# Performance work log

Hardware: AMD Instinct MI355X
Metric: run time of the kernel (lower is better)

The kernel has to match this reference:

```python
import jax, jax.numpy as jnp
import numpy as np

B, T, D, H, HD = 4, 2048, 1024, 16, 64
EPS = 1e-6


def _rotary_tables(seq_len, d_head):
    n = d_head // 4
    angular_freq = (1.0 / 1024) ** jnp.linspace(0, 1, n, dtype=jnp.float32)
    angular_freq = jnp.concatenate([angular_freq, jnp.zeros((n,), jnp.float32)])  # [d_head//2]
    theta = jnp.outer(jnp.arange(seq_len, dtype=jnp.float32), angular_freq)  # [T, d_head//2]
    return jnp.cos(theta), jnp.sin(theta)


def _apply_rotary(x, cos, sin):
    # x: [B, T, H, d]
    xf = x.astype(jnp.float32)
    x1, x2 = jnp.split(xf, 2, axis=-1)
    c = cos[None, :, None, :]
    s = sin[None, :, None, :]
    y1 = x1 * c + x2 * s
    y2 = -x1 * s + x2 * c
    return jnp.concatenate([y1, y2], axis=-1).astype(x.dtype)


def _rmsnorm(x, eps):
    return x * jax.lax.rsqrt(jnp.mean(x * x, axis=-1, keepdims=True) + eps)


def setup_inputs() -> dict:
    key = jax.random.key(0)
    ks = jax.random.split(key, 5)
    scale = 1.0 / np.sqrt(D)
    x = jax.random.normal(ks[0], (B, T, D), jnp.float32)
    wq = jax.random.normal(ks[1], (D, D), jnp.float32) * scale
    wk = jax.random.normal(ks[2], (D, D), jnp.float32) * scale
    wv = jax.random.normal(ks[3], (D, D), jnp.float32) * scale
    wo = jax.random.normal(ks[4], (D, D), jnp.float32) * scale
    mask = jnp.tril(jnp.ones((T, T), dtype=bool))  # causal
    return {"x": x, "wq": wq, "wk": wk, "wv": wv, "wo": wo, "mask": mask}


def reference(x, wq, wk, wv, wo, mask):
    # QKV projections (equinox Linear: y = x @ W.T)
    q = (x @ wq.T).reshape(B, T, H, HD)
    k = (x @ wk.T).reshape(B, T, H, HD)
    v = (x @ wv.T).reshape(B, T, H, HD)
    # QK-norm (RMS norm without weight)
    q = _rmsnorm(q, EPS)
    k = _rmsnorm(k, EPS)
    # Rotary embedding
    cos, sin = _rotary_tables(T, HD)
    q = _apply_rotary(q, cos, sin)
    k = _apply_rotary(k, cos, sin)
    # Attention
    scores = jnp.einsum('bshd,bthd->bhst', q, k) / jnp.sqrt(jnp.float32(HD))
    scores = jnp.where(mask[None, None, :, :], scores, -jnp.inf)
    weights = jax.nn.softmax(scores, axis=-1)
    out = jnp.einsum('bhst,bthd->bshd', weights, v)
    out = out.reshape(B, T, D)
    return out @ wo.T
```

## Files before the change

kernel.cpp:

```cpp
#include <hip/hip_runtime.h>
#include <hip/hip_bf16.h>
#include <math.h>

#define B_ 4
#define T_ 2048
#define D_ 1024
#define H_ 16
#define HD_ 64

typedef _Float16 f16x8 __attribute__((ext_vector_type(8)));
typedef _Float16 f16x4 __attribute__((ext_vector_type(4)));
typedef float f32x4 __attribute__((ext_vector_type(4)));

__device__ __forceinline__ void gload_lds16(const _Float16* g, _Float16* l) {
    __builtin_amdgcn_global_load_lds(
        (const __attribute__((address_space(1))) void*)g,
        (__attribute__((address_space(3))) void*)l,
        16, 0, 0);
}

__global__ __launch_bounds__(256) void castf(const float* __restrict__ in,
                                             _Float16* __restrict__ out, int n4) {
    const int i = blockIdx.x * 256 + threadIdx.x;
    if (i < n4) {
        const float4 v = ((const float4*)in)[i];
        f16x4 h = {(_Float16)v.x, (_Float16)v.y, (_Float16)v.z, (_Float16)v.w};
        ((f16x4*)out)[i] = h;
    }
}

__global__ __launch_bounds__(256) void castw(const float* __restrict__ a,
                                             const float* __restrict__ b,
                                             const float* __restrict__ c,
                                             const float* __restrict__ d,
                                             _Float16* __restrict__ oa,
                                             _Float16* __restrict__ ob,
                                             _Float16* __restrict__ oc,
                                             _Float16* __restrict__ od) {
    const int z = blockIdx.z;
    const float* in = (z == 0) ? a : (z == 1 ? b : (z == 2 ? c : d));
    _Float16* out = (z == 0) ? oa : (z == 1 ? ob : (z == 2 ? oc : od));
    const int i = blockIdx.x * 256 + threadIdx.x;
    const float4 v = ((const float4*)in)[i];
    f16x4 h = {(_Float16)v.x, (_Float16)v.y, (_Float16)v.z, (_Float16)v.w};
    ((f16x4*)out)[i] = h;
}

__global__ __launch_bounds__(256) void gemm_qkv(const _Float16* __restrict__ A,
                                                const _Float16* __restrict__ Wq,
                                                const _Float16* __restrict__ Wk,
                                                const _Float16* __restrict__ Wv,
                                                _Float16* __restrict__ qh,
                                                _Float16* __restrict__ kh,
                                                _Float16* __restrict__ vt) {
    constexpr int K = D_;
    const int z = blockIdx.z;
    const _Float16* W = (z == 0) ? Wq : (z == 1 ? Wk : Wv);
    __shared__ _Float16 As[128 * 32];
    __shared__ _Float16 Bs[128 * 32];
    const int tid = threadIdx.x;
    const int lane = tid & 63, w = tid >> 6;
    const int col = lane & 15, quad = lane >> 4;
    const int wm = w >> 1, wn = w & 1;
    const int row0 = blockIdx.x * 128, col0 = blockIdx.y * 128;
    const int sr = lane >> 2, sc = (lane & 3) * 8;

    f32x4 acc[4][4];
#pragma unroll
    for (int i = 0; i < 4; ++i)
#pragma unroll
        for (int j = 0; j < 4; ++j) acc[i][j] = (f32x4){0.f, 0.f, 0.f, 0.f};

    for (int kt = 0; kt < K / 32; ++kt) {
        const int k0 = kt * 32;
#pragma unroll
        for (int it = 0; it < 2; ++it) {
            const int rb = it * 64 + w * 16;
            gload_lds16(A + (size_t)(row0 + rb + sr) * K + k0 + sc, As + rb * 32);
            gload_lds16(W + (size_t)(col0 + rb + sr) * K + k0 + sc, Bs + rb * 32);
        }
        __syncthreads();
        f16x8 af[4], bf[4];
#pragma unroll
        for (int i = 0; i < 4; ++i) {
            af[i] = *(const f16x8*)&As[(wm * 64 + i * 16 + col) * 32 + quad * 8];
            bf[i] = *(const f16x8*)&Bs[(wn * 64 + i * 16 + col) * 32 + quad * 8];
        }
#pragma unroll
        for (int mi = 0; mi < 4; ++mi)
#pragma unroll
            for (int ni = 0; ni < 4; ++ni)
                acc[mi][ni] = __builtin_amdgcn_mfma_f32_16x16x32_f16(af[mi], bf[ni],
                                                                     acc[mi][ni], 0, 0, 0);
        __syncthreads();
    }

    if (z < 2) {
        _Float16* C = (z == 0) ? qh : kh;
        const float qscale = (z == 0) ? 0.18033688011112042f : 1.0f;
        const float fr = exp2f(-10.0f * (float)col * (1.0f / 15.0f));
#pragma unroll
        for (int mi = 0; mi < 4; ++mi) {
            float ssq[4];
#pragma unroll
            for (int r = 0; r < 4; ++r) {
                float t = 0.f;
#pragma unroll
                for (int ni = 0; ni < 4; ++ni) t += acc[mi][ni][r] * acc[mi][ni][r];
                ssq[r] = t;
            }
#pragma unroll
            for (int st = 1; st < 16; st <<= 1)
#pragma unroll
                for (int r = 0; r < 4; ++r) ssq[r] += __shfl_xor(ssq[r], st, 64);
            const int rowb = row0 + wm * 64 + mi * 16 + quad * 4;
#pragma unroll
            for (int r = 0; r < 4; ++r) {
                const float scl = rsqrtf(ssq[r] * (1.0f / 64.0f) + 1e-6f) * qscale;
                const int t = (rowb + r) & (T_ - 1);
                float s, c;
                __sincosf((float)t * fr, &s, &c);
                const float x0 = acc[mi][0][r] * scl;
                const float x1 = acc[mi][1][r] * scl;
                const float x2 = acc[mi][2][r] * scl;
                const float x3 = acc[mi][3][r] * scl;
                const float y0 = fmaf(x0, c, x2 * s);
                const float y2 = fmaf(x2, c, -x0 * s);
                const size_t base = (size_t)(rowb + r) * D_ + col0 + wn * 64 + col;
                C[base + 0]  = (_Float16)y0;
                C[base + 16] = (_Float16)x1;
                C[base + 32] = (_Float16)y2;
                C[base + 48] = (_Float16)x3;
            }
        }
    } else {
        const int hh = blockIdx.y * 2 + wn;
#pragma unroll
        for (int mi = 0; mi < 4; ++mi) {
            const int row = row0 + wm * 64 + mi * 16 + quad * 4;
            const int bb = row >> 11;
            const int t0m = row & (T_ - 1);
#pragma unroll
            for (int ni = 0; ni < 4; ++ni) {
                const int d = ni * 16 + col;
                f16x4 pk = {(_Float16)acc[mi][ni][0], (_Float16)acc[mi][ni][1],
                            (_Float16)acc[mi][ni][2], (_Float16)acc[mi][ni][3]};
                *(f16x4*)&vt[((size_t)(bb * H_ + hh) * HD_ + d) * T_ + t0m] = pk;
            }
        }
    }
}

__global__ __launch_bounds__(256) void gemm_wo(const _Float16* __restrict__ A,
                                               const _Float16* __restrict__ W,
                                               float* __restrict__ C) {
    constexpr int K = D_, N = D_;
    __shared__ _Float16 As[128 * 32];
    __shared__ _Float16 Bs[128 * 32];
    const int tid = threadIdx.x;
    const int lane = tid & 63, w = tid >> 6;
    const int col = lane & 15, quad = lane >> 4;
    const int wm = w >> 1, wn = w & 1;
    const int row0 = blockIdx.x * 128, col0 = blockIdx.y * 128;
    const int sr = lane >> 2, sc = (lane & 3) * 8;

    f32x4 acc[4][4];
#pragma unroll
    for (int i = 0; i < 4; ++i)
#pragma unroll
        for (int j = 0; j < 4; ++j) acc[i][j] = (f32x4){0.f, 0.f, 0.f, 0.f};

    for (int kt = 0; kt < K / 32; ++kt) {
        const int k0 = kt * 32;
#pragma unroll
        for (int it = 0; it < 2; ++it) {
            const int rb = it * 64 + w * 16;
            gload_lds16(A + (size_t)(row0 + rb + sr) * K + k0 + sc, As + rb * 32);
            gload_lds16(W + (size_t)(col0 + rb + sr) * K + k0 + sc, Bs + rb * 32);
        }
        __syncthreads();
        f16x8 af[4], bf[4];
#pragma unroll
        for (int i = 0; i < 4; ++i) {
            af[i] = *(const f16x8*)&As[(wm * 64 + i * 16 + col) * 32 + quad * 8];
            bf[i] = *(const f16x8*)&Bs[(wn * 64 + i * 16 + col) * 32 + quad * 8];
        }
#pragma unroll
        for (int mi = 0; mi < 4; ++mi)
#pragma unroll
            for (int ni = 0; ni < 4; ++ni)
                acc[mi][ni] = __builtin_amdgcn_mfma_f32_16x16x32_f16(af[mi], bf[ni],
                                                                     acc[mi][ni], 0, 0, 0);
        __syncthreads();
    }
#pragma unroll
    for (int mi = 0; mi < 4; ++mi)
#pragma unroll
        for (int ni = 0; ni < 4; ++ni)
#pragma unroll
            for (int r = 0; r < 4; ++r)
                C[(size_t)(row0 + wm * 64 + mi * 16 + quad * 4 + r) * N +
                  col0 + wn * 64 + ni * 16 + col] = acc[mi][ni][r];
}

#define LDP 88

__global__ __launch_bounds__(512) void flash_mfma(const _Float16* __restrict__ qh,
                                                  const _Float16* __restrict__ kh,
                                                  const _Float16* __restrict__ vt,
                                                  _Float16* __restrict__ o) {
    __shared__ _Float16 Kl[2][64 * 64];
    __shared__ _Float16 Vl[2][64 * 64];
    __shared__ _Float16 Pl[8][16 * LDP];
    const int tid = threadIdx.x;
    const int lane = tid & 63, w = tid >> 6;
    const int col = lane & 15, quad = lane >> 4;
    const int bh = blockIdx.x, b = bh >> 4, h = bh & 15;
    const int srow = lane >> 3;
    const int schunk = (lane & 7) ^ srow;
    const int sw = col & 7;
    const int sr = w * 8 + srow;
    const _Float16* kbase = kh + ((size_t)(b * T_ + sr) * H_ + h) * HD_ + schunk * 8;
    const _Float16* vbase = vt + ((size_t)(b * H_ + h) * HD_ + sr) * T_ + schunk * 8;

    for (int phase = 0; phase < 2; ++phase) {
        const int qt = (phase == 0) ? (int)blockIdx.y : (15 - (int)blockIdx.y);
        const int q0 = qt * 128;

        const int tq = q0 + w * 16 + col;
        const _Float16* qp = qh + ((size_t)(b * T_ + tq) * H_ + h) * HD_ + quad * 8;
        const f16x8 qB0 = *(const f16x8*)(qp);
        const f16x8 qB1 = *(const f16x8*)(qp + 32);

        f32x4 oa[4];
#pragma unroll
        for (int i = 0; i < 4; ++i) oa[i] = (f32x4){0.f, 0.f, 0.f, 0.f};
        float l_ = 0.f;

        const int nkt = 2 * qt + 2;
        gload_lds16(kbase, Kl[0] + (w * 8) * 64);
        gload_lds16(vbase, Vl[0] + (w * 8) * 64);

        for (int kt = 0; kt < nkt; ++kt) {
            const int cur = kt & 1;
            __syncthreads();
            if (kt + 1 < nkt) {
                const int k1 = (kt + 1) * 64;
                gload_lds16(kbase + (size_t)k1 * D_, Kl[cur ^ 1] + (w * 8) * 64);
                gload_lds16(vbase + k1, Vl[cur ^ 1] + (w * 8) * 64);
            }
            const int k0 = kt * 64;

            f32x4 s[4];
#pragma unroll
            for (int tn = 0; tn < 4; ++tn) {
                const _Float16* kp = &Kl[cur][(tn * 16 + col) * 64];
                const f16x8 kA0 = *(const f16x8*)(kp + ((quad ^ sw) << 3));
                const f16x8 kA1 = *(const f16x8*)(kp + (((quad | 4) ^ sw) << 3));
                f32x4 a = (f32x4){0.f, 0.f, 0.f, 0.f};
                a = __builtin_amdgcn_mfma_f32_16x16x32_f16(kA0, qB0, a, 0, 0, 0);
                a = __builtin_amdgcn_mfma_f32_16x16x32_f16(kA1, qB1, a, 0, 0, 0);
                s[tn] = a;
            }

            if (k0 + 63 > q0 + w * 16) {
                const int qq = q0 + w * 16 + col;
#pragma unroll
                for (int tn = 0; tn < 4; ++tn)
#pragma unroll
                    for (int r = 0; r < 4; ++r) {
                        const int key = k0 + tn * 16 + quad * 4 + r;
                        if (key > qq) s[tn][r] = -1e30f;
                    }
            }

#pragma unroll
            for (int tn = 0; tn < 4; ++tn) {
                f16x4 pk;
#pragma unroll
                for (int r = 0; r < 4; ++r) {
                    const float p = exp2f(s[tn][r]);
                    l_ += p;
                    pk[r] = (_Float16)p;
                }
                *(f16x4*)&Pl[w][col * LDP + tn * 16 + quad * 4] = pk;
            }

            const f16x8 pA0 = *(const f16x8*)&Pl[w][col * LDP + quad * 8];
            const f16x8 pA1 = *(const f16x8*)&Pl[w][col * LDP + quad * 8 + 32];
#pragma unroll
            for (int tn = 0; tn < 4; ++tn) {
                const _Float16* vp = &Vl[cur][(tn * 16 + col) * 64];
                const f16x8 vB0 = *(const f16x8*)(vp + ((quad ^ sw) << 3));
                const f16x8 vB1 = *(const f16x8*)(vp + (((quad | 4) ^ sw) << 3));
                oa[tn] = __builtin_amdgcn_mfma_f32_16x16x32_f16(pA0, vB0, oa[tn], 0, 0, 0);
                oa[tn] = __builtin_amdgcn_mfma_f32_16x16x32_f16(pA1, vB1, oa[tn], 0, 0, 0);
            }
        }
        __syncthreads();

        l_ += __shfl_xor(l_, 16, 64);
        l_ += __shfl_xor(l_, 32, 64);
        const float linv = 1.0f / l_;
        float inv[4];
#pragma unroll
        for (int r = 0; r < 4; ++r) inv[r] = __shfl(linv, quad * 4 + r, 64);
#pragma unroll
        for (int tn = 0; tn < 4; ++tn)
#pragma unroll
            for (int r = 0; r < 4; ++r)
                o[((size_t)(b * T_ + q0 + w * 16 + quad * 4 + r) * H_ + h) * HD_ + tn * 16 + col] =
                    (_Float16)(oa[tn][r] * inv[r]);
    }
}

extern "C" void kernel_launch(void* const* d_in, const int* in_sizes, int n_in,
                              void* d_out, int out_size, void* d_ws, size_t ws_size,
                              hipStream_t stream) {
    const float* x  = (const float*)d_in[0];
    const float* wq = (const float*)d_in[1];
    const float* wk = (const float*)d_in[2];
    const float* wv = (const float*)d_in[3];
    const float* wo = (const float*)d_in[4];
    float* out = (float*)d_out;

    const size_t NE = (size_t)B_ * T_ * D_;
    const size_t WE = (size_t)D_ * D_;
    _Float16* xh  = (_Float16*)d_ws;
    _Float16* qh  = xh + NE;
    _Float16* kh  = qh + NE;
    _Float16* vth = kh + NE;
    _Float16* oh  = vth + NE;
    _Float16* wqh = oh + NE;
    _Float16* wkh = wqh + WE;
    _Float16* wvh = wkh + WE;
    _Float16* woh = wvh + WE;

    castf<<<NE / 1024, 256, 0, stream>>>(x, xh, (int)(NE / 4));
    castw<<<dim3(WE / 1024, 1, 4), 256, 0, stream>>>(wq, wk, wv, wo,
                                                     wqh, wkh, wvh, woh);

    gemm_qkv<<<dim3((B_ * T_) / 128, D_ / 128, 3), 256, 0, stream>>>(
        xh, wqh, wkh, wvh, qh, kh, vth);

    flash_mfma<<<dim3(B_ * H_, 8, 1), 512, 0, stream>>>(qh, kh, vth, oh);

    gemm_wo<<<dim3((B_ * T_) / 128, D_ / 128, 1), 256, 0, stream>>>(oh, woh, out);
}
```

Measured before the change: 280.5 us.

## Restructure flash attention to 4 waves with 32 query rows each

The flash kernel moves from 512-thread blocks, each processing two paired causal query tiles, to 256-thread blocks that each own one 128-row query tile, launched longest-first. Each wave now computes two 16-row query sub-tiles, so every K/V fragment read from LDS feeds twice as many MFMAs. The double-buffered K/V prefetch is dropped for a single buffer loaded and synchronised each iteration. The intent is more data reuse per LDS read and more blocks per CU, at the cost of losing load/compute overlap within a block and of the paired-tile load balancing.

```diff
diff --git a/kernel.cpp b/kernel.cpp
--- a/kernel.cpp
+++ b/kernel.cpp
@@ -205,113 +205,134 @@
 
 #define LDP 88
 
-__global__ __launch_bounds__(512) void flash_mfma(const _Float16* __restrict__ qh,
+__global__ __launch_bounds__(256) void flash_mfma(const _Float16* __restrict__ qh,
                                                   const _Float16* __restrict__ kh,
                                                   const _Float16* __restrict__ vt,
                                                   _Float16* __restrict__ o) {
-    __shared__ _Float16 Kl[2][64 * 64];
-    __shared__ _Float16 Vl[2][64 * 64];
-    __shared__ _Float16 Pl[8][16 * LDP];
+    __shared__ _Float16 Kl[64 * 64];
+    __shared__ _Float16 Vl[64 * 64];
+    __shared__ _Float16 Pl[4][32 * LDP];
     const int tid = threadIdx.x;
     const int lane = tid & 63, w = tid >> 6;
     const int col = lane & 15, quad = lane >> 4;
     const int bh = blockIdx.x, b = bh >> 4, h = bh & 15;
+    const int qt = 15 - (int)blockIdx.y;
+    const int q0 = qt * 128;
     const int srow = lane >> 3;
-    const int schunk = (lane & 7) ^ srow;
+    const int schunk = ((lane & 7) ^ srow) * 8;
     const int sw = col & 7;
-    const int sr = w * 8 + srow;
-    const _Float16* kbase = kh + ((size_t)(b * T_ + sr) * H_ + h) * HD_ + schunk * 8;
-    const _Float16* vbase = vt + ((size_t)(b * H_ + h) * HD_ + sr) * T_ + schunk * 8;
-
-    for (int phase = 0; phase < 2; ++phase) {
-        const int qt = (phase == 0) ? (int)blockIdx.y : (15 - (int)blockIdx.y);
-        const int q0 = qt * 128;
-
-        const int tq = q0 + w * 16 + col;
-        const _Float16* qp = qh + ((size_t)(b * T_ + tq) * H_ + h) * HD_ + quad * 8;
-        const f16x8 qB0 = *(const f16x8*)(qp);
-        const f16x8 qB1 = *(const f16x8*)(qp + 32);
-
-        f32x4 oa[4];
-#pragma unroll
-        for (int i = 0; i < 4; ++i) oa[i] = (f32x4){0.f, 0.f, 0.f, 0.f};
-        float l_ = 0.f;
-
-        const int nkt = 2 * qt + 2;
-        gload_lds16(kbase, Kl[0] + (w * 8) * 64);
-        gload_lds16(vbase, Vl[0] + (w * 8) * 64);
-
-        for (int kt = 0; kt < nkt; ++kt) {
-            const int cur = kt & 1;
-            __syncthreads();
-            if (kt + 1 < nkt) {
-                const int k1 = (kt + 1) * 64;
-                gload_lds16(kbase + (size_t)k1 * D_, Kl[cur ^ 1] + (w * 8) * 64);
-                gload_lds16(vbase + k1, Vl[cur ^ 1] + (w * 8) * 64);
+
+    const int qa = q0 + w * 32 + col;
+    const _Float16* qpa = qh + ((size_t)(b * T_ + qa) * H_ + h) * HD_ + quad * 8;
+    const f16x8 qB0a = *(const f16x8*)(qpa);
+    const f16x8 qB1a = *(const f16x8*)(qpa + 32);
+    const _Float16* qpb = qpa + (size_t)16 * D_;
+    const f16x8 qB0b = *(const f16x8*)(qpb);
+    const f16x8 qB1b = *(const f16x8*)(qpb + 32);
+
+    f32x4 oaa[4], oab[4];
+#pragma unroll
+    for (int i = 0; i < 4; ++i) {
+        oaa[i] = (f32x4){0.f, 0.f, 0.f, 0.f};
+        oab[i] = (f32x4){0.f, 0.f, 0.f, 0.f};
+    }
+    float la = 0.f, lb = 0.f;
+
+    const int nkt = 2 * qt + 2;
+    for (int kt = 0; kt < nkt; ++kt) {
+        const int k0 = kt * 64;
+#pragma unroll
+        for (int half = 0; half < 2; ++half) {
+            const int r = half * 32 + w * 8 + srow;
+            gload_lds16(kh + ((size_t)(b * T_ + k0 + r) * H_ + h) * HD_ + schunk,
+                        Kl + (half * 32 + w * 8) * 64);
+            gload_lds16(vt + ((size_t)(b * H_ + h) * HD_ + r) * T_ + k0 + schunk,
+                        Vl + (half * 32 + w * 8) * 64);
+        }
+        __syncthreads();
+
+        f32x4 sa[4], sb[4];
+#pragma unroll
+        for (int tn = 0; tn < 4; ++tn) {
+            const _Float16* kp = &Kl[(tn * 16 + col) * 64];
+            const f16x8 kA0 = *(const f16x8*)(kp + ((quad ^ sw) << 3));
+            const f16x8 kA1 = *(const f16x8*)(kp + (((quad | 4) ^ sw) << 3));
+            f32x4 xa = (f32x4){0.f, 0.f, 0.f, 0.f};
+            f32x4 xb = (f32x4){0.f, 0.f, 0.f, 0.f};
+            xa = __builtin_amdgcn_mfma_f32_16x16x32_f16(kA0, qB0a, xa, 0, 0, 0);
+            xb = __builtin_amdgcn_mfma_f32_16x16x32_f16(kA0, qB0b, xb, 0, 0, 0);
+            xa = __builtin_amdgcn_mfma_f32_16x16x32_f16(kA1, qB1a, xa, 0, 0, 0);
+            xb = __builtin_amdgcn_mfma_f32_16x16x32_f16(kA1, qB1b, xb, 0, 0, 0);
+            sa[tn] = xa;
+            sb[tn] = xb;
+        }
+
+        if (k0 + 63 > q0 + w * 32) {
+#pragma unroll
+            for (int tn = 0; tn < 4; ++tn)
+#pragma unroll
+                for (int r = 0; r < 4; ++r) {
+                    const int key = k0 + tn * 16 + quad * 4 + r;
+                    if (key > qa) sa[tn][r] = -1e30f;
+                    if (key > qa + 16) sb[tn][r] = -1e30f;
+                }
+        }
+
+#pragma unroll
+        for (int tn = 0; tn < 4; ++tn) {
+            f16x4 pka, pkb;
+#pragma unroll
+            for (int r = 0; r < 4; ++r) {
+                const float pa = exp2f(sa[tn][r]);
+                const float pb = exp2f(sb[tn][r]);
+                la += pa;
+                lb += pb;
+                pka[r] = (_Float16)pa;
+                pkb[r] = (_Float16)pb;
             }
-            const int k0 = kt * 64;
-
-            f32x4 s[4];
-#pragma unroll
-            for (int tn = 0; tn < 4; ++tn) {
-                const _Float16* kp = &Kl[cur][(tn * 16 + col) * 64];
-                const f16x8 kA0 = *(const f16x8*)(kp + ((quad ^ sw) << 3));
-                const f16x8 kA1 = *(const f16x8*)(kp + (((quad | 4) ^ sw) << 3));
-                f32x4 a = (f32x4){0.f, 0.f, 0.f, 0.f};
-                a = __builtin_amdgcn_mfma_f32_16x16x32_f16(kA0, qB0, a, 0, 0, 0);
-                a = __builtin_amdgcn_mfma_f32_16x16x32_f16(kA1, qB1, a, 0, 0, 0);
-                s[tn] = a;
-            }
-
-            if (k0 + 63 > q0 + w * 16) {
-                const int qq = q0 + w * 16 + col;
-#pragma unroll
-                for (int tn = 0; tn < 4; ++tn)
-#pragma unroll
-                    for (int r = 0; r < 4; ++r) {
-                        const int key = k0 + tn * 16 + quad * 4 + r;
-                        if (key > qq) s[tn][r] = -1e30f;
-                    }
-            }
-
-#pragma unroll
-            for (int tn = 0; tn < 4; ++tn) {
-                f16x4 pk;
-#pragma unroll
-                for (int r = 0; r < 4; ++r) {
-                    const float p = exp2f(s[tn][r]);
-                    l_ += p;
-                    pk[r] = (_Float16)p;
-                }
-                *(f16x4*)&Pl[w][col * LDP + tn * 16 + quad * 4] = pk;
-            }
-
-            const f16x8 pA0 = *(const f16x8*)&Pl[w][col * LDP + quad * 8];
-            const f16x8 pA1 = *(const f16x8*)&Pl[w][col * LDP + quad * 8 + 32];
-#pragma unroll
-            for (int tn = 0; tn < 4; ++tn) {
-                const _Float16* vp = &Vl[cur][(tn * 16 + col) * 64];
-                const f16x8 vB0 = *(const f16x8*)(vp + ((quad ^ sw) << 3));
-                const f16x8 vB1 = *(const f16x8*)(vp + (((quad | 4) ^ sw) << 3));
-                oa[tn] = __builtin_amdgcn_mfma_f32_16x16x32_f16(pA0, vB0, oa[tn], 0, 0, 0);
-                oa[tn] = __builtin_amdgcn_mfma_f32_16x16x32_f16(pA1, vB1, oa[tn], 0, 0, 0);
-            }
-        }
-        __syncthreads();
-
-        l_ += __shfl_xor(l_, 16, 64);
-        l_ += __shfl_xor(l_, 32, 64);
-        const float linv = 1.0f / l_;
-        float inv[4];
-#pragma unroll
-        for (int r = 0; r < 4; ++r) inv[r] = __shfl(linv, quad * 4 + r, 64);
-#pragma unroll
-        for (int tn = 0; tn < 4; ++tn)
-#pragma unroll
-            for (int r = 0; r < 4; ++r)
-                o[((size_t)(b * T_ + q0 + w * 16 + quad * 4 + r) * H_ + h) * HD_ + tn * 16 + col] =
-                    (_Float16)(oa[tn][r] * inv[r]);
-    }
+            *(f16x4*)&Pl[w][col * LDP + tn * 16 + quad * 4] = pka;
+            *(f16x4*)&Pl[w][(col + 16) * LDP + tn * 16 + quad * 4] = pkb;
+        }
+
+        const f16x8 pA0a = *(const f16x8*)&Pl[w][col * LDP + quad * 8];
+        const f16x8 pA1a = *(const f16x8*)&Pl[w][col * LDP + quad * 8 + 32];
+        const f16x8 pA0b = *(const f16x8*)&Pl[w][(col + 16) * LDP + quad * 8];
+        const f16x8 pA1b = *(const f16x8*)&Pl[w][(col + 16) * LDP + quad * 8 + 32];
+#pragma unroll
+        for (int tn = 0; tn < 4; ++tn) {
+            const _Float16* vp = &Vl[(tn * 16 + col) * 64];
+            const f16x8 vB0 = *(const f16x8*)(vp + ((quad ^ sw) << 3));
+            const f16x8 vB1 = *(const f16x8*)(vp + (((quad | 4) ^ sw) << 3));
+            oaa[tn] = __builtin_amdgcn_mfma_f32_16x16x32_f16(pA0a, vB0, oaa[tn], 0, 0, 0);
+            oab[tn] = __builtin_amdgcn_mfma_f32_16x16x32_f16(pA0b, vB0, oab[tn], 0, 0, 0);
+            oaa[tn] = __builtin_amdgcn_mfma_f32_16x16x32_f16(pA1a, vB1, oaa[tn], 0, 0, 0);
+            oab[tn] = __builtin_amdgcn_mfma_f32_16x16x32_f16(pA1b, vB1, oab[tn], 0, 0, 0);
+        }
+        __syncthreads();
+    }
+
+    la += __shfl_xor(la, 16, 64);
+    la += __shfl_xor(la, 32, 64);
+    lb += __shfl_xor(lb, 16, 64);
+    lb += __shfl_xor(lb, 32, 64);
+    const float linva = 1.0f / la;
+    const float linvb = 1.0f / lb;
+    float inva[4], invb[4];
+#pragma unroll
+    for (int r = 0; r < 4; ++r) {
+        inva[r] = __shfl(linva, quad * 4 + r, 64);
+        invb[r] = __shfl(linvb, quad * 4 + r, 64);
+    }
+    const int qrow = q0 + w * 32 + quad * 4;
+#pragma unroll
+    for (int tn = 0; tn < 4; ++tn)
+#pragma unroll
+        for (int r = 0; r < 4; ++r) {
+            o[((size_t)(b * T_ + qrow + r) * H_ + h) * HD_ + tn * 16 + col] =
+                (_Float16)(oaa[tn][r] * inva[r]);
+            o[((size_t)(b * T_ + qrow + 16 + r) * H_ + h) * HD_ + tn * 16 + col] =
+                (_Float16)(oab[tn][r] * invb[r]);
+        }
 }
 
 extern "C" void kernel_launch(void* const* d_in, const int* in_sizes, int n_in,
@@ -343,7 +364,7 @@
     gemm_qkv<<<dim3((B_ * T_) / 128, D_ / 128, 3), 256, 0, stream>>>(
         xh, wqh, wkh, wvh, qh, kh, vth);
 
-    flash_mfma<<<dim3(B_ * H_, 8, 1), 512, 0, stream>>>(qh, kh, vth, oh);
+    flash_mfma<<<dim3(B_ * H_, 16, 1), 256, 0, stream>>>(qh, kh, vth, oh);
 
     gemm_wo<<<dim3((B_ * T_) / 128, D_ / 128, 1), 256, 0, stream>>>(oh, woh, out);
 }
```

New measurement: 279.8 us. Within noise of the previous version (-0.3%).
